# Performance work log

Measured on AMD Instinct MI355X. Metric: run time of the kernel, lower is better.

Reference implementation:

```python
import jax, jax.numpy as jnp
import numpy as np

H = W = 512; CELL = 8; P = 16; GX = GY = 64; NGH = GX // 2
SHIFTS = ((0, 0), (1, 0), (0, 1), (1, 1))
EPS = 1e-8
TWO_PI = 2.0 * np.pi

def _diff_round(x):
    return x - jnp.sin(x * TWO_PI) / TWO_PI

def _harder_diff_round(x):
    return _diff_round(_diff_round(x))

def _patches(pad_arr, sx, sy):
    # pad_arr: (H+2*CELL, W+2*CELL, C) -> (NGH*NGH, P, P, C) overlapping supervoxel patches
    x0 = sx * CELL + CELL - (P - CELL) // 2
    y0 = sy * CELL + CELL - (P - CELL) // 2
    s = pad_arr[x0:x0 + NGH * P, y0:y0 + NGH * P]
    c = s.shape[-1]
    return s.reshape(NGH, P, NGH, P, c).transpose(0, 2, 1, 3, 4).reshape(NGH * NGH, P, P, c)

def _conv_trio(x, w, b):
    y = jax.lax.conv_general_dilated(x, w, (1, 1), 'SAME', dimension_numbers=('NHWC', 'HWIO', 'NHWC'))
    return jax.nn.relu(y + b)

def _mlp(x, w0, b0, w1, b1, w2, b2, w3, b3):
    # mlp_features=[5,5,5] with relu, final linear projection to latent_size=10
    x = jax.nn.relu(x @ w0 + b0)
    x = jax.nn.relu(x @ w1 + b1)
    x = jax.nn.relu(x @ w2 + b2)
    return x @ w3 + b3

def _forward(curr_image, curr_label, masks, conv1_w, conv1_b, conv2_w, conv2_b, dense1_w, dense1_b,
             we0, be0, we1, be1, we2, be2, we3, be3, wn0, bn0, wn1, bn1, wn2, bn2, wn3, bn3,
             wout, bout, senders, receivers):
    ids = jnp.arange(GX * GY, dtype=masks.dtype).reshape(GX, GY)
    img, lab, msk = curr_image[0], curr_label[0], masks[0]
    pad_img = jnp.pad(img, ((CELL, CELL), (CELL, CELL), (0, 0)))
    pad_lab = jnp.pad(lab, ((CELL, CELL), (CELL, CELL), (0, 0)))
    pad_msk = jnp.pad(msk[..., None], ((CELL, CELL), (CELL, CELL), (0, 0)), constant_values=-1.0)
    toks, lsv = [], []
    for sx, sy in SHIFTS:  # fixed 4 shift groups (structural, not data loop)
        cid = ids[sx::2, sy::2].reshape(-1)                                    # (F,)
        filt = (_patches(pad_msk, sx, sy)[..., 0] == cid[:, None, None]).astype(img.dtype)  # (F,P,P)
        toks.append(_patches(pad_img, sx, sy) * filt[..., None])              # masked image patches
        lp = _patches(pad_lab, sx, sy)[..., 0]
        summ = jnp.sum(filt, axis=(1, 2))
        lsv.append(_harder_diff_round(jnp.sum(lp * filt, axis=(1, 2)) / (summ + EPS)))
    tokens = jnp.concatenate(toks, axis=0)      # (N, P, P, 1), N = GX*GY
    label_svs = jnp.concatenate(lsv, axis=0)    # (N,)
    x = _conv_trio(tokens, conv1_w, conv1_b)
    x = _conv_trio(x, conv2_w, conv2_b)
    nodes = jax.nn.relu(x.reshape(x.shape[0], -1) @ dense1_w + dense1_b)      # (N, 6)
    n = nodes.shape[0]; e = senders.shape[0]
    ones_e = jnp.ones((e, 1), nodes.dtype)      # broadcast global context [[1]]
    edge_feat = _mlp(jnp.concatenate([nodes[senders], nodes[receivers], ones_e], -1),
                     we0, be0, we1, be1, we2, be2, we3, be3)                   # (E, 10)
    agg = jax.ops.segment_sum(edge_feat, receivers, num_segments=n)            # (N, 10)
    ones_n = jnp.ones((n, 1), nodes.dtype)
    new_nodes = _mlp(jnp.concatenate([nodes, agg, ones_n], -1),
                     wn0, bn0, wn1, bn1, wn2, bn2, wn3, bn3)                   # (N, 10)
    logits = new_nodes @ wout + bout                                           # (N, 2)
    labels2 = jnp.stack([1.0 - label_svs, label_svs], axis=-1)
    return -jnp.sum(labels2 * jax.nn.log_softmax(logits, axis=-1), axis=-1)    # (N,)

def setup_inputs():
    key = jax.random.key(0)
    ks = jax.random.split(key, 32)
    def w(i, shape):
        fan = int(np.prod(shape[:-1]))
        return jax.random.normal(ks[i], shape, jnp.float32) / np.sqrt(fan)
    curr_image = jax.random.normal(ks[0], (1, H, W, 1), jnp.float32)
    curr_label = (jax.random.uniform(ks[1], (1, H, W, 1)) > 0.5).astype(jnp.float32)
    # masks: per-pixel supervoxel id = id of containing 8x8 grid cell
    ids = np.arange(GX * GY, dtype=np.float32).reshape(GX, GY)
    masks = jnp.asarray(np.repeat(np.repeat(ids, CELL, 0), CELL, 1))[None]  # (1, H, W)
    # node index consistent with group-concatenation order of tokens
    node_id = np.zeros((GX, GY), dtype=np.int32)
    for g, (sx, sy) in enumerate(SHIFTS):
        node_id[sx::2, sy::2] = g * NGH * NGH + np.arange(NGH * NGH, dtype=np.int32).reshape(NGH, NGH)
    a = node_id[:, :-1].ravel(); b = node_id[:, 1:].ravel()
    c = node_id[:-1, :].ravel(); d = node_id[1:, :].ravel()
    senders = jnp.asarray(np.concatenate([a, b, c, d]))     # (16128,)
    receivers = jnp.asarray(np.concatenate([b, a, d, c]))
    return dict(curr_image=curr_image, curr_label=curr_label, masks=masks,
                conv1_w=w(2, (3, 3, 1, 40)), conv1_b=jnp.zeros((40,), jnp.float32),
                conv2_w=w(3, (3, 3, 40, 40)), conv2_b=jnp.zeros((40,), jnp.float32),
                dense1_w=w(4, (P * P * 40, 6)), dense1_b=jnp.zeros((6,), jnp.float32),
                we0=w(5, (13, 5)), be0=jnp.zeros((5,), jnp.float32),
                we1=w(6, (5, 5)), be1=jnp.zeros((5,), jnp.float32),
                we2=w(7, (5, 5)), be2=jnp.zeros((5,), jnp.float32),
                we3=w(8, (5, 10)), be3=jnp.zeros((10,), jnp.float32),
                wn0=w(9, (17, 5)), bn0=jnp.zeros((5,), jnp.float32),
                wn1=w(10, (5, 5)), bn1=jnp.zeros((5,), jnp.float32),
                wn2=w(11, (5, 5)), bn2=jnp.zeros((5,), jnp.float32),
                wn3=w(12, (5, 10)), bn3=jnp.zeros((10,), jnp.float32),
                wout=w(13, (10, 2)), bout=jnp.zeros((2,), jnp.float32),
                senders=senders, receivers=receivers)

def reference(curr_image, curr_label, masks, conv1_w, conv1_b, conv2_w, conv2_b, dense1_w, dense1_b,
              we0, be0, we1, be1, we2, be2, we3, be3, wn0, bn0, wn1, bn1, wn2, bn2, wn3, bn3,
              wout, bout, senders, receivers):
    return _forward(curr_image, curr_label, masks, conv1_w, conv1_b, conv2_w, conv2_b, dense1_w, dense1_b,
                    we0, be0, we1, be1, we2, be2, we3, be3, wn0, bn0, wn1, bn1, wn2, bn2, wn3, bn3,
                    wout, bout, senders, receivers)
```

## Files before the change

### kernel.cpp

```cpp
#include <hip/hip_runtime.h>
#include <math.h>


typedef __attribute__((ext_vector_type(8))) short short8;
typedef __attribute__((ext_vector_type(4))) float f32x4;

#define ZROW  324
#define NWTB  (12 * 4 * 48 * 8)
#define ND1W  (256 * 40 * 6)
#define ND1P  64

static __device__ __forceinline__ unsigned short f2bf(float x) {
    unsigned int u = __float_as_uint(x);
    u += 0x7FFF + ((u >> 16) & 1);
    return (unsigned short)(u >> 16);
}

static __device__ __forceinline__ float diff_round(float x) {
    const float TP = 6.2831853071795864769f;
    return x - sinf(x * TP) / TP;
}

template<int IN, int OUT>
static __device__ __forceinline__ void mlp_layer(const float* in,
                                                 const float* __restrict__ w,
                                                 const float* __restrict__ b,
                                                 float* out, bool do_relu) {
#pragma unroll
    for (int j = 0; j < OUT; ++j) {
        float a = b[j];
#pragma unroll
        for (int i = 0; i < IN; ++i) a = fmaf(in[i], w[i * OUT + j], a);
        out[j] = do_relu ? fmaxf(a, 0.f) : a;
    }
}

__global__ __launch_bounds__(256) void k_prep(const float* __restrict__ w2,
                                              const float* __restrict__ d1w,
                                              unsigned short* __restrict__ wTbG,
                                              unsigned short* __restrict__ d1wb) {
    const int i = blockIdx.x * 256 + threadIdx.x;
    if (i < NWTB) {
        const int j    = i & 7;
        const int co   = (i >> 3) % 48;
        const int qg   = (i >> 3) / 48;
        const int quad = qg & 3;
        const int grp  = qg >> 2;
        float val = 0.f;
        if (grp < 9) {
            if (co < 40) val = w2[(grp * 40 + quad * 8 + j) * 40 + co];
        } else {
            const int tap = (grp - 9) * 4 + quad;
            if (tap < 9 && co < 40) val = w2[(tap * 40 + 32 + j) * 40 + co];
        }
        wTbG[i] = f2bf(val);
    } else if (i < NWTB + ND1W + ND1P) {
        const int jj = i - NWTB;
        if (jj < ND1W) {
            const int k  = jj % 6;
            const int co = (jj / 6) % 40;
            const int px = (jj / 6) / 40;
            d1wb[jj] = f2bf(d1w[(px * 40 + co) * 6 + k]);
        } else {
            d1wb[jj] = 0;
        }
    }
}

__global__ __launch_bounds__(512, 4) void k_patch(
    const float* __restrict__ img, const float* __restrict__ lab,
    const float* __restrict__ msk,
    const float* __restrict__ w1, const float* __restrict__ b1,
    const unsigned short* __restrict__ wTbG,
    const float* __restrict__ b2,
    const unsigned short* __restrict__ d1wb, const float* __restrict__ d1b,
    float* __restrict__ nodes, float* __restrict__ lsv)
{
    __shared__ __align__(16) unsigned short x1[325 * 40];
    __shared__ __align__(16) unsigned short Bs[NWTB];
    __shared__ float p[256];
    __shared__ float red[4][2];
    __shared__ float wsum[8][6];

    const int n = blockIdx.x;
    const int t = threadIdx.x;
    const int g = n >> 10, cell = n & 1023;
    const int gi = cell >> 5, gj = cell & 31;
    const int sx = g & 1, sy = g >> 1;
    const int gx = sx + 2 * gi, gy = sy + 2 * gj;
    const int px0 = gx * 8 - 4, py0 = gy * 8 - 4;
    const float cid = (float)(gx * 64 + gy);

    const int ph = t >> 8, pix = t & 255;
    const int u = pix >> 4, v = pix & 15;
    const int lane = t & 63, wv = t >> 6;
    const int lane15 = t & 15, quad = (t >> 4) & 3;

    float m = -1.f, iv = 0.f, lv = 0.f;
    if (ph == 0) {
        const int r = px0 + u, c = py0 + v;
        if (r >= 0 && r < 512 && c >= 0 && c < 512) {
            m  = msk[r * 512 + c];
            iv = img[r * 512 + c];
            lv = lab[r * 512 + c];
        }
    }

    {
        const uint4* src = (const uint4*)wTbG;
        uint4* dst = (uint4*)Bs;
        for (int i = t; i < NWTB / 8; i += 512) dst[i] = src[i];
    }

    {
        unsigned int* x1w = (unsigned int*)x1;
        for (int i = t; i < 69 * 20; i += 512) {
            const int cellI = i / 20, d = i - cellI * 20;
            int cr;
            if      (cellI < 18) cr = cellI;
            else if (cellI < 36) cr = cellI + 288;
            else if (cellI < 52) cr = (cellI - 35) * 18;
            else if (cellI < 68) cr = (cellI - 51) * 18 + 17;
            else                 cr = ZROW;
            x1w[cr * 20 + d] = 0u;
        }
    }

    const float f = (m == cid) ? 1.f : 0.f;
    if (ph == 0) {
        p[pix] = iv * f;
        float sf = f, slf = lv * f;
        for (int off = 32; off; off >>= 1) {
            sf  += __shfl_down(sf,  off);
            slf += __shfl_down(slf, off);
        }
        if (lane == 0) { red[wv][0] = sf; red[wv][1] = slf; }
    }
    __syncthreads();

    if (t == 0) {
        const float SF = red[0][0] + red[1][0] + red[2][0] + red[3][0];
        const float SL = red[0][1] + red[1][1] + red[2][1] + red[3][1];
        lsv[n] = diff_round(diff_round(SL / (SF + 1e-8f)));
    }

    {
        float nbv[9];
#pragma unroll
        for (int ky = 0; ky < 3; ++ky)
#pragma unroll
            for (int kx = 0; kx < 3; ++kx) {
                const int uy = u + ky - 1, vx = v + kx - 1;
                const bool ok = (uy >= 0) && (uy < 16) && (vx >= 0) && (vx < 16);
                nbv[ky * 3 + kx] = ok ? p[uy * 16 + vx] : 0.f;
            }
        float a1[20];
#pragma unroll
        for (int cc = 0; cc < 20; ++cc) a1[cc] = b1[ph * 20 + cc];
#pragma unroll
        for (int k = 0; k < 9; ++k) {
            const float xv = nbv[k];
#pragma unroll
            for (int cc = 0; cc < 20; ++cc)
                a1[cc] = fmaf(xv, w1[k * 40 + ph * 20 + cc], a1[cc]);
        }
        const int row = (u + 1) * 18 + (v + 1);
        unsigned int* x1w = (unsigned int*)x1;
#pragma unroll
        for (int cg = 0; cg < 10; ++cg) {
            const unsigned int lo = f2bf(fmaxf(a1[2 * cg], 0.f));
            const unsigned int hi = f2bf(fmaxf(a1[2 * cg + 1], 0.f));
            x1w[row * 20 + ph * 10 + cg] = lo | (hi << 16);
        }
    }
    __syncthreads();

    float bias[3];
#pragma unroll
    for (int nt = 0; nt < 3; ++nt) {
        const int co = nt * 16 + lane15;
        bias[nt] = (co < 40) ? b2[co] : 0.f;
    }
    f32x4 acc[2][3];
#pragma unroll
    for (int mt = 0; mt < 2; ++mt)
#pragma unroll
        for (int nt = 0; nt < 3; ++nt) {
            acc[mt][nt][0] = bias[nt]; acc[mt][nt][1] = bias[nt];
            acc[mt][nt][2] = bias[nt]; acc[mt][nt][3] = bias[nt];
        }

#pragma unroll
    for (int tap = 0; tap < 9; ++tap) {
        const int ky = tap / 3, kx = tap % 3;
        short8 bf[3];
#pragma unroll
        for (int nt = 0; nt < 3; ++nt)
            bf[nt] = *(const short8*)(Bs + ((tap * 4 + quad) * 48 + nt * 16 + lane15) * 8);
#pragma unroll
        for (int mt = 0; mt < 2; ++mt) {
            const int arow = (wv * 2 + mt + ky) * 18 + (lane15 + kx);
            const short8 a0 = *(const short8*)(x1 + arow * 40 + quad * 8);
#pragma unroll
            for (int nt = 0; nt < 3; ++nt)
                acc[mt][nt] = __builtin_amdgcn_mfma_f32_16x16x32_bf16(
                    a0, bf[nt], acc[mt][nt], 0, 0, 0);
        }
    }
#pragma unroll
    for (int s = 0; s < 3; ++s) {
        short8 bt[3];
#pragma unroll
        for (int nt = 0; nt < 3; ++nt)
            bt[nt] = *(const short8*)(Bs + (((9 + s) * 4 + quad) * 48 + nt * 16 + lane15) * 8);
        const int tapq = s * 4 + quad;
        const int kyq  = (tapq * 11) >> 5;
        const int kxq  = tapq - 3 * kyq;
#pragma unroll
        for (int mt = 0; mt < 2; ++mt) {
            const int arowq = (wv * 2 + mt + kyq) * 18 + (lane15 + kxq);
            const int offs  = (tapq < 9) ? (arowq * 40 + 32) : (ZROW * 40);
            const short8 at = *(const short8*)(x1 + offs);
#pragma unroll
            for (int nt = 0; nt < 3; ++nt)
                acc[mt][nt] = __builtin_amdgcn_mfma_f32_16x16x32_bf16(
                    at, bt[nt], acc[mt][nt], 0, 0, 0);
        }
    }

    const unsigned int* d1u = (const unsigned int*)d1wb;
    float a6[6] = {0.f, 0.f, 0.f, 0.f, 0.f, 0.f};
#pragma unroll
    for (int mt = 0; mt < 2; ++mt)
#pragma unroll
        for (int nt = 0; nt < 3; ++nt) {
            const int co = nt * 16 + lane15;
#pragma unroll
            for (int reg = 0; reg < 4; ++reg) {
                const int pixel = (wv * 2 + mt) * 16 + quad * 4 + reg;
                const int dwb = (pixel * 40 + co) * 3;
                const unsigned int w0  = d1u[dwb];
                const unsigned int w1v = d1u[dwb + 1];
                const unsigned int w2v = d1u[dwb + 2];
                const float a = fmaxf(acc[mt][nt][reg], 0.f);
                a6[0] = fmaf(a, __uint_as_float(w0 << 16),           a6[0]);
                a6[1] = fmaf(a, __uint_as_float(w0 & 0xFFFF0000u),   a6[1]);
                a6[2] = fmaf(a, __uint_as_float(w1v << 16),          a6[2]);
                a6[3] = fmaf(a, __uint_as_float(w1v & 0xFFFF0000u),  a6[3]);
                a6[4] = fmaf(a, __uint_as_float(w2v << 16),          a6[4]);
                a6[5] = fmaf(a, __uint_as_float(w2v & 0xFFFF0000u),  a6[5]);
            }
        }
    for (int off = 32; off; off >>= 1) {
#pragma unroll
        for (int k = 0; k < 6; ++k) a6[k] += __shfl_down(a6[k], off);
    }
    if (lane == 0) {
#pragma unroll
        for (int k = 0; k < 6; ++k) wsum[wv][k] = a6[k];
    }
    __syncthreads();
    if (t < 6) {
        float s = d1b[t];
#pragma unroll
        for (int w = 0; w < 8; ++w) s += wsum[w][t];
        nodes[n * 6 + t] = fmaxf(s, 0.f);
    }
}


#define OWE0 0
#define OBE0 65
#define OWE1 70
#define OBE1 95
#define OWE2 100
#define OBE2 125
#define OWE3 130
#define OBE3 180
#define OWN0 190
#define OBN0 275
#define OWN1 280
#define OBN1 305
#define OWN2 310
#define OBN2 335
#define OWN3 340
#define OBN3 390
#define OWOUT 400
#define OBOUT 420
#define NWPOOL 422

__global__ __launch_bounds__(64) void k_node(
    const float* __restrict__ nodes, const float* __restrict__ lsv,
    const float* __restrict__ we0, const float* __restrict__ be0,
    const float* __restrict__ we1, const float* __restrict__ be1,
    const float* __restrict__ we2, const float* __restrict__ be2,
    const float* __restrict__ we3, const float* __restrict__ be3,
    const float* __restrict__ wn0, const float* __restrict__ bn0,
    const float* __restrict__ wn1, const float* __restrict__ bn1,
    const float* __restrict__ wn2, const float* __restrict__ bn2,
    const float* __restrict__ wn3, const float* __restrict__ bn3,
    const float* __restrict__ wout, const float* __restrict__ bout,
    float* __restrict__ out, int N)
{
    __shared__ float L[NWPOOL];
    const int t = threadIdx.x;

    {
        const float* srcs[18] = {we0, be0, we1, be1, we2, be2, we3, be3,
                                 wn0, bn0, wn1, bn1, wn2, bn2, wn3, bn3,
                                 wout, bout};
        const int lens[18] = {65, 5, 25, 5, 25, 5, 50, 10,
                              85, 5, 25, 5, 25, 5, 50, 10, 20, 2};
        int off = 0;
        for (int a = 0; a < 18; ++a) {
            for (int i = t; i < lens[a]; i += 64) L[off + i] = srcs[a][i];
            off += lens[a];
        }
    }
    __syncthreads();

    const int n = blockIdx.x * 16 + (t >> 2);
    const int d = t & 3;
    const bool nvalid = n < N;

    const int g = n >> 10, cell = n & 1023;
    const int gi = cell >> 5, gj = cell & 31;
    const int gx = (g & 1) + 2 * gi, gy = (g >> 1) + 2 * gj;

    float self6[6];
#pragma unroll
    for (int i = 0; i < 6; ++i) self6[i] = nvalid ? nodes[n * 6 + i] : 0.f;

    const int DX[4] = {0, 0, -1, 1};
    const int DY[4] = {-1, 1, 0, 0};
    const int x = gx + DX[d], y = gy + DY[d];
    const bool ev = nvalid && x >= 0 && x < 64 && y >= 0 && y < 64;

    float o10[10];
#pragma unroll
    for (int j = 0; j < 10; ++j) o10[j] = 0.f;
    if (ev) {
        const int mid = ((x & 1) + 2 * (y & 1)) * 1024 + (x >> 1) * 32 + (y >> 1);
        float in13[13];
#pragma unroll
        for (int i = 0; i < 6; ++i) in13[i] = nodes[mid * 6 + i];
#pragma unroll
        for (int i = 0; i < 6; ++i) in13[6 + i] = self6[i];
        in13[12] = 1.f;
        float h0[5], h1[5], h2[5];
        mlp_layer<13, 5>(in13, L + OWE0, L + OBE0, h0, true);
        mlp_layer<5, 5>(h0, L + OWE1, L + OBE1, h1, true);
        mlp_layer<5, 5>(h1, L + OWE2, L + OBE2, h2, true);
        mlp_layer<5, 10>(h2, L + OWE3, L + OBE3, o10, false);
    }

    float agg[10];
#pragma unroll
    for (int j = 0; j < 10; ++j) {
        float v = o10[j];
        v += __shfl_xor(v, 1);
        v += __shfl_xor(v, 2);
        agg[j] = v;
    }

    float in17[17];
#pragma unroll
    for (int i = 0; i < 6; ++i)  in17[i]     = self6[i];
#pragma unroll
    for (int i = 0; i < 10; ++i) in17[6 + i] = agg[i];
    in17[16] = 1.f;
    float h0[5], h1[5], h2[5], o[10];
    mlp_layer<17, 5>(in17, L + OWN0, L + OBN0, h0, true);
    mlp_layer<5, 5>(h0, L + OWN1, L + OBN1, h1, true);
    mlp_layer<5, 5>(h1, L + OWN2, L + OBN2, h2, true);
    mlp_layer<5, 10>(h2, L + OWN3, L + OBN3, o, false);

    float l0 = L[OBOUT + 0], l1 = L[OBOUT + 1];
#pragma unroll
    for (int i = 0; i < 10; ++i) {
        l0 = fmaf(o[i], L[OWOUT + i * 2 + 0], l0);
        l1 = fmaf(o[i], L[OWOUT + i * 2 + 1], l1);
    }
    if (d == 0 && nvalid) {
        const float mx  = fmaxf(l0, l1);
        const float e0  = expf(l0 - mx), e1 = expf(l1 - mx);
        const float lse = mx + logf(e0 + e1);
        const float sv  = lsv[n];
        out[n] = -((1.f - sv) * (l0 - lse) + sv * (l1 - lse));
    }
}

extern "C" void kernel_launch(void* const* d_in, const int* in_sizes, int n_in,
                              void* d_out, int out_size, void* d_ws, size_t ws_size,
                              hipStream_t stream) {
    (void)n_in; (void)ws_size; (void)in_sizes;
    const float* img = (const float*)d_in[0];
    const float* lab = (const float*)d_in[1];
    const float* msk = (const float*)d_in[2];
    const float* w1  = (const float*)d_in[3];
    const float* b1  = (const float*)d_in[4];
    const float* w2  = (const float*)d_in[5];
    const float* b2  = (const float*)d_in[6];
    const float* d1w = (const float*)d_in[7];
    const float* d1b = (const float*)d_in[8];
    const float* we0 = (const float*)d_in[9],  *be0 = (const float*)d_in[10];
    const float* we1 = (const float*)d_in[11], *be1 = (const float*)d_in[12];
    const float* we2 = (const float*)d_in[13], *be2 = (const float*)d_in[14];
    const float* we3 = (const float*)d_in[15], *be3 = (const float*)d_in[16];
    const float* wn0 = (const float*)d_in[17], *bn0 = (const float*)d_in[18];
    const float* wn1 = (const float*)d_in[19], *bn1 = (const float*)d_in[20];
    const float* wn2 = (const float*)d_in[21], *bn2 = (const float*)d_in[22];
    const float* wn3 = (const float*)d_in[23], *bn3 = (const float*)d_in[24];
    const float* wout = (const float*)d_in[25], *bout = (const float*)d_in[26];
    const int N = out_size;

    char* base = (char*)d_ws;
    float* nodes = (float*)base;
    float* lsvb  = (float*)(base + (size_t)N * 6 * 4);
    unsigned short* wTbG = (unsigned short*)(base + (size_t)N * 7 * 4);
    unsigned short* d1wb = wTbG + NWTB;
    float* out   = (float*)d_out;

    const int prep_n = NWTB + ND1W + ND1P;
    k_prep<<<(prep_n + 255) / 256, 256, 0, stream>>>(w2, d1w, wTbG, d1wb);
    k_patch<<<N, 512, 0, stream>>>(img, lab, msk, w1, b1, wTbG, b2,
                                   d1wb, d1b, nodes, lsvb);
    k_node<<<(N + 15) / 16, 64, 0, stream>>>(nodes, lsvb,
                                             we0, be0, we1, be1, we2, be2,
                                             we3, be3,
                                             wn0, bn0, wn1, bn1, wn2, bn2,
                                             wn3, bn3, wout, bout, out, N);
}
```

Measured before the change: 221.0 us.

## Split fused patch kernel into conv1 and half-patch conv2 kernels via global buffer

When the workspace is large enough, the fused per-patch kernel is split into a conv1 kernel that writes bf16 activations to global memory and a conv2 kernel that processes each patch in two halves with 256-thread blocks and a smaller shared weight tile. Partial dense sums from the halves are combined in the node kernel, which now applies the dense bias and ReLU. The aim is higher occupancy and more parallelism in the MFMA stage by cutting per-block LDS use. In exchange it adds a global round trip of about 100 MB of activations and an extra launch.

```diff
diff --git a/kernel.cpp b/kernel.cpp
--- a/kernel.cpp
+++ b/kernel.cpp
@@ -7,8 +7,10 @@
 
 #define ZROW  324
 #define NWTB  (12 * 4 * 48 * 8)
+#define NWMB  (9 * 4 * 48 * 8)
 #define ND1W  (256 * 40 * 6)
 #define ND1P  64
+#define X1PS  13000
 
 static __device__ __forceinline__ unsigned short f2bf(float x) {
     unsigned int u = __float_as_uint(x);
@@ -67,20 +69,14 @@
     }
 }
 
-__global__ __launch_bounds__(512, 4) void k_patch(
+__global__ __launch_bounds__(512, 4) void k_conv1(
     const float* __restrict__ img, const float* __restrict__ lab,
     const float* __restrict__ msk,
     const float* __restrict__ w1, const float* __restrict__ b1,
-    const unsigned short* __restrict__ wTbG,
-    const float* __restrict__ b2,
-    const unsigned short* __restrict__ d1wb, const float* __restrict__ d1b,
-    float* __restrict__ nodes, float* __restrict__ lsv)
+    unsigned short* __restrict__ x1g, float* __restrict__ lsv)
 {
-    __shared__ __align__(16) unsigned short x1[325 * 40];
-    __shared__ __align__(16) unsigned short Bs[NWTB];
     __shared__ float p[256];
     __shared__ float red[4][2];
-    __shared__ float wsum[8][6];
 
     const int n = blockIdx.x;
     const int t = threadIdx.x;
@@ -94,7 +90,8 @@
     const int ph = t >> 8, pix = t & 255;
     const int u = pix >> 4, v = pix & 15;
     const int lane = t & 63, wv = t >> 6;
-    const int lane15 = t & 15, quad = (t >> 4) & 3;
+
+    unsigned int* x1w = (unsigned int*)x1g + (size_t)n * (X1PS / 2);
 
     float m = -1.f, iv = 0.f, lv = 0.f;
     if (ph == 0) {
@@ -106,12 +103,224 @@
         }
     }
 
+    for (int i = t; i < 69 * 20; i += 512) {
+        const int cellI = i / 20, d = i - cellI * 20;
+        int cr;
+        if      (cellI < 18) cr = cellI;
+        else if (cellI < 36) cr = cellI + 288;
+        else if (cellI < 52) cr = (cellI - 35) * 18;
+        else if (cellI < 68) cr = (cellI - 51) * 18 + 17;
+        else                 cr = ZROW;
+        x1w[cr * 20 + d] = 0u;
+    }
+
+    const float f = (m == cid) ? 1.f : 0.f;
+    if (ph == 0) {
+        p[pix] = iv * f;
+        float sf = f, slf = lv * f;
+        for (int off = 32; off; off >>= 1) {
+            sf  += __shfl_down(sf,  off);
+            slf += __shfl_down(slf, off);
+        }
+        if (lane == 0) { red[wv][0] = sf; red[wv][1] = slf; }
+    }
+    __syncthreads();
+
+    if (t == 0) {
+        const float SF = red[0][0] + red[1][0] + red[2][0] + red[3][0];
+        const float SL = red[0][1] + red[1][1] + red[2][1] + red[3][1];
+        lsv[n] = diff_round(diff_round(SL / (SF + 1e-8f)));
+    }
+
+    {
+        float nbv[9];
+#pragma unroll
+        for (int ky = 0; ky < 3; ++ky)
+#pragma unroll
+            for (int kx = 0; kx < 3; ++kx) {
+                const int uy = u + ky - 1, vx = v + kx - 1;
+                const bool ok = (uy >= 0) && (uy < 16) && (vx >= 0) && (vx < 16);
+                nbv[ky * 3 + kx] = ok ? p[uy * 16 + vx] : 0.f;
+            }
+        float a1[20];
+#pragma unroll
+        for (int cc = 0; cc < 20; ++cc) a1[cc] = b1[ph * 20 + cc];
+#pragma unroll
+        for (int k = 0; k < 9; ++k) {
+            const float xv = nbv[k];
+#pragma unroll
+            for (int cc = 0; cc < 20; ++cc)
+                a1[cc] = fmaf(xv, w1[k * 40 + ph * 20 + cc], a1[cc]);
+        }
+        const int row = (u + 1) * 18 + (v + 1);
+#pragma unroll
+        for (int cg = 0; cg < 10; ++cg) {
+            const unsigned int lo = f2bf(fmaxf(a1[2 * cg], 0.f));
+            const unsigned int hi = f2bf(fmaxf(a1[2 * cg + 1], 0.f));
+            x1w[row * 20 + ph * 10 + cg] = lo | (hi << 16);
+        }
+    }
+}
+
+__global__ __launch_bounds__(256, 5) void k_conv2(
+    const unsigned short* __restrict__ x1g,
+    const unsigned short* __restrict__ wTbG,
+    const float* __restrict__ b2,
+    const unsigned short* __restrict__ d1wb,
+    float* __restrict__ P)
+{
+    __shared__ __align__(16) unsigned short Bs[NWMB];
+    __shared__ float wsum[4][6];
+
+    const int bid = blockIdx.x;
+    const int n = bid >> 1, h = bid & 1;
+    const int t = threadIdx.x;
+    const int lane = t & 63, wv = t >> 6;
+    const int lane15 = t & 15, quad = (t >> 4) & 3;
+
+    {
+        const uint4* src = (const uint4*)wTbG;
+        uint4* dst = (uint4*)Bs;
+        for (int i = t; i < NWMB / 8; i += 256) dst[i] = src[i];
+    }
+    __syncthreads();
+
+    const unsigned short* x1 = x1g + (size_t)n * X1PS;
+
+    float bias[3];
+#pragma unroll
+    for (int nt = 0; nt < 3; ++nt) {
+        const int co = nt * 16 + lane15;
+        bias[nt] = (co < 40) ? b2[co] : 0.f;
+    }
+    f32x4 acc[2][3];
+#pragma unroll
+    for (int mt = 0; mt < 2; ++mt)
+#pragma unroll
+        for (int nt = 0; nt < 3; ++nt) {
+            acc[mt][nt][0] = bias[nt]; acc[mt][nt][1] = bias[nt];
+            acc[mt][nt][2] = bias[nt]; acc[mt][nt][3] = bias[nt];
+        }
+
+#pragma unroll
+    for (int tap = 0; tap < 9; ++tap) {
+        const int ky = tap / 3, kx = tap % 3;
+        short8 bf[3];
+#pragma unroll
+        for (int nt = 0; nt < 3; ++nt)
+            bf[nt] = *(const short8*)(Bs + ((tap * 4 + quad) * 48 + nt * 16 + lane15) * 8);
+#pragma unroll
+        for (int mt = 0; mt < 2; ++mt) {
+            const int arow = (h * 8 + wv * 2 + mt + ky) * 18 + (lane15 + kx);
+            const short8 a0 = *(const short8*)(x1 + arow * 40 + quad * 8);
+#pragma unroll
+            for (int nt = 0; nt < 3; ++nt)
+                acc[mt][nt] = __builtin_amdgcn_mfma_f32_16x16x32_bf16(
+                    a0, bf[nt], acc[mt][nt], 0, 0, 0);
+        }
+    }
+#pragma unroll
+    for (int s = 0; s < 3; ++s) {
+        short8 bt[3];
+#pragma unroll
+        for (int nt = 0; nt < 3; ++nt)
+            bt[nt] = *(const short8*)(wTbG + (((9 + s) * 4 + quad) * 48 + nt * 16 + lane15) * 8);
+        const int tapq = s * 4 + quad;
+        const int kyq  = (tapq * 11) >> 5;
+        const int kxq  = tapq - 3 * kyq;
+#pragma unroll
+        for (int mt = 0; mt < 2; ++mt) {
+            const int arowq = (h * 8 + wv * 2 + mt + kyq) * 18 + (lane15 + kxq);
+            const int offs  = (tapq < 9) ? (arowq * 40 + 32) : (ZROW * 40);
+            const short8 at = *(const short8*)(x1 + offs);
+#pragma unroll
+            for (int nt = 0; nt < 3; ++nt)
+                acc[mt][nt] = __builtin_amdgcn_mfma_f32_16x16x32_bf16(
+                    at, bt[nt], acc[mt][nt], 0, 0, 0);
+        }
+    }
+
+    const unsigned int* d1u = (const unsigned int*)d1wb;
+    float a6[6] = {0.f, 0.f, 0.f, 0.f, 0.f, 0.f};
+#pragma unroll
+    for (int mt = 0; mt < 2; ++mt)
+#pragma unroll
+        for (int nt = 0; nt < 3; ++nt) {
+            const int co = nt * 16 + lane15;
+#pragma unroll
+            for (int reg = 0; reg < 4; ++reg) {
+                const int pixel = (h * 8 + wv * 2 + mt) * 16 + quad * 4 + reg;
+                const int dwb = (pixel * 40 + co) * 3;
+                const unsigned int w0  = d1u[dwb];
+                const unsigned int w1v = d1u[dwb + 1];
+                const unsigned int w2v = d1u[dwb + 2];
+                const float a = fmaxf(acc[mt][nt][reg], 0.f);
+                a6[0] = fmaf(a, __uint_as_float(w0 << 16),           a6[0]);
+                a6[1] = fmaf(a, __uint_as_float(w0 & 0xFFFF0000u),   a6[1]);
+                a6[2] = fmaf(a, __uint_as_float(w1v << 16),          a6[2]);
+                a6[3] = fmaf(a, __uint_as_float(w1v & 0xFFFF0000u),  a6[3]);
+                a6[4] = fmaf(a, __uint_as_float(w2v << 16),          a6[4]);
+                a6[5] = fmaf(a, __uint_as_float(w2v & 0xFFFF0000u),  a6[5]);
+            }
+        }
+    for (int off = 32; off; off >>= 1) {
+#pragma unroll
+        for (int k = 0; k < 6; ++k) a6[k] += __shfl_down(a6[k], off);
+    }
+    if (lane == 0) {
+#pragma unroll
+        for (int k = 0; k < 6; ++k) wsum[wv][k] = a6[k];
+    }
+    __syncthreads();
+    if (t < 6) {
+        float s = wsum[0][t] + wsum[1][t] + wsum[2][t] + wsum[3][t];
+        P[(n * 2 + h) * 6 + t] = s;
+    }
+}
+
+__global__ __launch_bounds__(512, 4) void k_patch(
+    const float* __restrict__ img, const float* __restrict__ lab,
+    const float* __restrict__ msk,
+    const float* __restrict__ w1, const float* __restrict__ b1,
+    const unsigned short* __restrict__ wTbG,
+    const float* __restrict__ b2,
+    const unsigned short* __restrict__ d1wb,
+    float* __restrict__ P, float* __restrict__ lsv)
+{
+    __shared__ __align__(16) unsigned short x1[325 * 40];
+    __shared__ __align__(16) unsigned short Bs[NWTB];
+    __shared__ float p[256];
+    __shared__ float red[4][2];
+    __shared__ float wsum[8][6];
+
+    const int n = blockIdx.x;
+    const int t = threadIdx.x;
+    const int g = n >> 10, cell = n & 1023;
+    const int gi = cell >> 5, gj = cell & 31;
+    const int sx = g & 1, sy = g >> 1;
+    const int gx = sx + 2 * gi, gy = sy + 2 * gj;
+    const int px0 = gx * 8 - 4, py0 = gy * 8 - 4;
+    const float cid = (float)(gx * 64 + gy);
+
+    const int ph = t >> 8, pix = t & 255;
+    const int u = pix >> 4, v = pix & 15;
+    const int lane = t & 63, wv = t >> 6;
+    const int lane15 = t & 15, quad = (t >> 4) & 3;
+
+    float m = -1.f, iv = 0.f, lv = 0.f;
+    if (ph == 0) {
+        const int r = px0 + u, c = py0 + v;
+        if (r >= 0 && r < 512 && c >= 0 && c < 512) {
+            m  = msk[r * 512 + c];
+            iv = img[r * 512 + c];
+            lv = lab[r * 512 + c];
+        }
+    }
     {
         const uint4* src = (const uint4*)wTbG;
         uint4* dst = (uint4*)Bs;
         for (int i = t; i < NWTB / 8; i += 512) dst[i] = src[i];
     }
-
     {
         unsigned int* x1w = (unsigned int*)x1;
         for (int i = t; i < 69 * 20; i += 512) {
@@ -125,7 +334,6 @@
             x1w[cr * 20 + d] = 0u;
         }
     }
-
     const float f = (m == cid) ? 1.f : 0.f;
     if (ph == 0) {
         p[pix] = iv * f;
@@ -137,13 +345,11 @@
         if (lane == 0) { red[wv][0] = sf; red[wv][1] = slf; }
     }
     __syncthreads();
-
     if (t == 0) {
         const float SF = red[0][0] + red[1][0] + red[2][0] + red[3][0];
         const float SL = red[0][1] + red[1][1] + red[2][1] + red[3][1];
         lsv[n] = diff_round(diff_round(SL / (SF + 1e-8f)));
     }
-
     {
         float nbv[9];
 #pragma unroll
@@ -189,7 +395,6 @@
             acc[mt][nt][0] = bias[nt]; acc[mt][nt][1] = bias[nt];
             acc[mt][nt][2] = bias[nt]; acc[mt][nt][3] = bias[nt];
         }
-
 #pragma unroll
     for (int tap = 0; tap < 9; ++tap) {
         const int ky = tap / 3, kx = tap % 3;
@@ -227,7 +432,6 @@
                     at, bt[nt], acc[mt][nt], 0, 0, 0);
         }
     }
-
     const unsigned int* d1u = (const unsigned int*)d1wb;
     float a6[6] = {0.f, 0.f, 0.f, 0.f, 0.f, 0.f};
 #pragma unroll
@@ -261,10 +465,11 @@
     }
     __syncthreads();
     if (t < 6) {
-        float s = d1b[t];
+        float s = 0.f;
 #pragma unroll
         for (int w = 0; w < 8; ++w) s += wsum[w][t];
-        nodes[n * 6 + t] = fmaxf(s, 0.f);
+        P[n * 12 + t]     = s;
+        P[n * 12 + 6 + t] = 0.f;
     }
 }
 
@@ -287,10 +492,12 @@
 #define OBN3 390
 #define OWOUT 400
 #define OBOUT 420
-#define NWPOOL 422
+#define OD1B 422
+#define NWPOOL 428
 
 __global__ __launch_bounds__(64) void k_node(
-    const float* __restrict__ nodes, const float* __restrict__ lsv,
+    const float* __restrict__ P, const float* __restrict__ lsv,
+    const float* __restrict__ d1b,
     const float* __restrict__ we0, const float* __restrict__ be0,
     const float* __restrict__ we1, const float* __restrict__ be1,
     const float* __restrict__ we2, const float* __restrict__ be2,
@@ -306,13 +513,13 @@
     const int t = threadIdx.x;
 
     {
-        const float* srcs[18] = {we0, be0, we1, be1, we2, be2, we3, be3,
+        const float* srcs[19] = {we0, be0, we1, be1, we2, be2, we3, be3,
                                  wn0, bn0, wn1, bn1, wn2, bn2, wn3, bn3,
-                                 wout, bout};
-        const int lens[18] = {65, 5, 25, 5, 25, 5, 50, 10,
-                              85, 5, 25, 5, 25, 5, 50, 10, 20, 2};
+                                 wout, bout, d1b};
+        const int lens[19] = {65, 5, 25, 5, 25, 5, 50, 10,
+                              85, 5, 25, 5, 25, 5, 50, 10, 20, 2, 6};
         int off = 0;
-        for (int a = 0; a < 18; ++a) {
+        for (int a = 0; a < 19; ++a) {
             for (int i = t; i < lens[a]; i += 64) L[off + i] = srcs[a][i];
             off += lens[a];
         }
@@ -329,7 +536,9 @@
 
     float self6[6];
 #pragma unroll
-    for (int i = 0; i < 6; ++i) self6[i] = nvalid ? nodes[n * 6 + i] : 0.f;
+    for (int i = 0; i < 6; ++i)
+        self6[i] = nvalid ? fmaxf(L[OD1B + i] + P[n * 12 + i] + P[n * 12 + 6 + i], 0.f)
+                          : 0.f;
 
     const int DX[4] = {0, 0, -1, 1};
     const int DY[4] = {-1, 1, 0, 0};
@@ -343,7 +552,8 @@
         const int mid = ((x & 1) + 2 * (y & 1)) * 1024 + (x >> 1) * 32 + (y >> 1);
         float in13[13];
 #pragma unroll
-        for (int i = 0; i < 6; ++i) in13[i] = nodes[mid * 6 + i];
+        for (int i = 0; i < 6; ++i)
+            in13[i] = fmaxf(L[OD1B + i] + P[mid * 12 + i] + P[mid * 12 + 6 + i], 0.f);
 #pragma unroll
         for (int i = 0; i < 6; ++i) in13[6 + i] = self6[i];
         in13[12] = 1.f;
@@ -393,7 +603,7 @@
 extern "C" void kernel_launch(void* const* d_in, const int* in_sizes, int n_in,
                               void* d_out, int out_size, void* d_ws, size_t ws_size,
                               hipStream_t stream) {
-    (void)n_in; (void)ws_size; (void)in_sizes;
+    (void)n_in; (void)in_sizes;
     const float* img = (const float*)d_in[0];
     const float* lab = (const float*)d_in[1];
     const float* msk = (const float*)d_in[2];
@@ -415,17 +625,40 @@
     const int N = out_size;
 
     char* base = (char*)d_ws;
-    float* nodes = (float*)base;
-    float* lsvb  = (float*)(base + (size_t)N * 6 * 4);
-    unsigned short* wTbG = (unsigned short*)(base + (size_t)N * 7 * 4);
-    unsigned short* d1wb = wTbG + NWTB;
-    float* out   = (float*)d_out;
+    const size_t X1G_B = (size_t)4096 * X1PS * 2;
+    const size_t P_B   = (size_t)4096 * 12 * 4;
+    const size_t LSV_B = (size_t)4096 * 4;
+    const size_t WTB_B = (size_t)NWTB * 2;
+    const size_t D1W_B = (size_t)(ND1W + ND1P) * 2;
+    const bool split = ws_size >= X1G_B + P_B + LSV_B + WTB_B + D1W_B;
+
+    unsigned short* x1g = nullptr;
+    float *P, *lsvb;
+    unsigned short *wTbG, *d1wb;
+    if (split) {
+        x1g  = (unsigned short*)base;
+        P    = (float*)(base + X1G_B);
+        lsvb = (float*)(base + X1G_B + P_B);
+        wTbG = (unsigned short*)(base + X1G_B + P_B + LSV_B);
+        d1wb = (unsigned short*)(base + X1G_B + P_B + LSV_B + WTB_B);
+    } else {
+        P    = (float*)base;
+        lsvb = (float*)(base + P_B);
+        wTbG = (unsigned short*)(base + P_B + LSV_B);
+        d1wb = (unsigned short*)(base + P_B + LSV_B + WTB_B);
+    }
+    float* out = (float*)d_out;
 
     const int prep_n = NWTB + ND1W + ND1P;
     k_prep<<<(prep_n + 255) / 256, 256, 0, stream>>>(w2, d1w, wTbG, d1wb);
-    k_patch<<<N, 512, 0, stream>>>(img, lab, msk, w1, b1, wTbG, b2,
-                                   d1wb, d1b, nodes, lsvb);
-    k_node<<<(N + 15) / 16, 64, 0, stream>>>(nodes, lsvb,
+    if (split) {
+        k_conv1<<<N, 512, 0, stream>>>(img, lab, msk, w1, b1, x1g, lsvb);
+        k_conv2<<<2 * N, 256, 0, stream>>>(x1g, wTbG, b2, d1wb, P);
+    } else {
+        k_patch<<<N, 512, 0, stream>>>(img, lab, msk, w1, b1, wTbG, b2,
+                                       d1wb, P, lsvb);
+    }
+    k_node<<<(N + 15) / 16, 64, 0, stream>>>(P, lsvb, d1b,
                                              we0, be0, we1, be1, we2, be2,
                                              we3, be3,
                                              wn0, bn0, wn1, bn1, wn2, bn2,
```

After: 272.5 us. 23.3% more time.
